# Kernel optimization log

Hardware: AMD Instinct MI355X
Metric: run time of the kernel (lower is better)

Reference implementation:

```python
import jax, jax.numpy as jnp
import numpy as np

B, LQ, LS, H = 4, 4096, 4096, 1024

def setup_inputs() -> dict:
    key = jax.random.key(0)
    k1, k2 = jax.random.split(key)
    query_input = jax.random.normal(k1, (B, LQ, H), dtype=jnp.float32)
    source_input = jax.random.normal(k2, (B, LS, H), dtype=jnp.float32)
    return {"query_input": query_input, "source_input": source_input}

def reference(query_input, source_input):
    # logits: [B, LQ, LS] = Q @ S^T, scaled by sqrt(d_k)
    dk = jnp.asarray(query_input.shape[-1], dtype=query_input.dtype)
    logits = jnp.einsum('bqh,bsh->bqs', query_input, source_input) / jnp.sqrt(dk)
    weights = jax.nn.softmax(logits, axis=-1)  # dropout inactive in eval mode
    # output: [B, LQ, H] = weights @ S (source doubles as values)
    return jnp.einsum('bqs,bsh->bqh', weights, source_input)
```

## Files before the change

### kernel.cpp

```cpp
#include <hip/hip_runtime.h>
#include <hip/hip_bf16.h>

#define B_   4
#define LQ_  4096
#define LS_  4096
#define DH_  1024
#define BQ_  64
#define BS_  256
#define NT_  (LS_/BS_)
#define NTH  512

typedef __bf16 bf16x8 __attribute__((ext_vector_type(8)));
typedef float  f32x4  __attribute__((ext_vector_type(4)));
typedef float  f32x16 __attribute__((ext_vector_type(16)));
typedef unsigned char u8;

#define WAITL()  asm volatile("s_waitcnt lgkmcnt(0)" ::: "memory")
#define BAR()    __builtin_amdgcn_s_barrier()

__device__ __forceinline__ unsigned short f2bf(float f) {
  union { __bf16 h; unsigned short u; } cv;
  cv.h = (__bf16)f;
  return cv.u;
}
__device__ __forceinline__ bf16x8 cvt8(f32x4 a, f32x4 b) {
  bf16x8 r;
  r[0] = (__bf16)a[0]; r[1] = (__bf16)a[1]; r[2] = (__bf16)a[2]; r[3] = (__bf16)a[3];
  r[4] = (__bf16)b[0]; r[5] = (__bf16)b[1]; r[6] = (__bf16)b[2]; r[7] = (__bf16)b[3];
  return r;
}

__global__ __launch_bounds__(256) void cvt_kernel(const float* __restrict__ S,
                                                  u8* __restrict__ Kf,
                                                  u8* __restrict__ Vf)
{
  __shared__ unsigned short tile[64][72];
  const int b  = blockIdx.z;
  const int dt = blockIdx.y;
  const int st = blockIdx.x;
  const int tid = threadIdx.x;
  const int t  = st >> 2;
  const float* Sbase = S + ((size_t)b*LS_ + (size_t)st*64)*DH_ + dt*64;

  #pragma unroll
  for (int k = 0; k < 4; ++k) {
    int fi  = tid + k*256;
    int row = fi >> 4;
    int c4  = fi & 15;
    float4 v = *reinterpret_cast<const float4*>(Sbase + (size_t)row*DH_ + c4*4);
    ushort4 h;
    h.x = f2bf(v.x); h.y = f2bf(v.y); h.z = f2bf(v.z); h.w = f2bf(v.w);
    *reinterpret_cast<ushort4*>(&tile[row][c4*4]) = h;
  }
  __syncthreads();

  #pragma unroll
  for (int h2 = 0; h2 < 2; ++h2) {
    int u    = tid + h2*256;
    int blk  = u >> 6;
    int wloc = blk >> 2;
    int kkl  = blk & 3;
    int lane = u & 63;
    int sh   = lane >> 5, sl = lane & 31;
    int srow = wloc*32 + sl;
    int scol = kkl*16 + sh*8;
    ushort4 h0 = *reinterpret_cast<const ushort4*>(&tile[srow][scol]);
    ushort4 h1 = *reinterpret_cast<const ushort4*>(&tile[srow][scol+4]);
    int w_g  = (st & 3)*2 + wloc;
    int kk_g = dt*4 + kkl;
    u8* dst = Kf + (size_t)(((b*16 + t)*8 + w_g)*64 + kk_g)*1024 + lane*16;
    *reinterpret_cast<ushort4*>(dst)     = h0;
    *reinterpret_cast<ushort4*>(dst + 8) = h1;
  }

  #pragma unroll
  for (int h2 = 0; h2 < 2; ++h2) {
    int u    = tid + h2*256;
    int blk  = u >> 6;
    int ksl  = blk >> 2;
    int nfl  = blk & 3;
    int lane = u & 63;
    int lg   = lane >> 4, lr = lane & 15;
    int srow = ksl*32 + lg*8;
    int dcol = nfl*16 + lr;
    ushort4 h0, h1;
    h0.x = tile[srow+0][dcol]; h0.y = tile[srow+1][dcol];
    h0.z = tile[srow+2][dcol]; h0.w = tile[srow+3][dcol];
    h1.x = tile[srow+4][dcol]; h1.y = tile[srow+5][dcol];
    h1.z = tile[srow+6][dcol]; h1.w = tile[srow+7][dcol];
    int w_g = dt >> 1;
    int i_g = ((st & 3)*2 + ksl)*8 + (dt & 1)*4 + nfl;
    u8* dst = Vf + (size_t)(((b*16 + t)*8 + w_g)*64 + i_g)*1024 + lane*16;
    *reinterpret_cast<ushort4*>(dst)     = h0;
    *reinterpret_cast<ushort4*>(dst + 8) = h1;
  }
}

__global__ __launch_bounds__(NTH, 2) void attn_kernel(
    const float* __restrict__ Qg,
    const u8* __restrict__ Kf,
    const u8* __restrict__ Vf,
    float* __restrict__ Og)
{
  __shared__ __align__(16) unsigned char qlds[131072];
  __shared__ __align__(16) unsigned char plds[32768];

  const int tid = threadIdx.x;
  const int w  = tid >> 6;
  const int l  = tid & 63;
  const int lg = l >> 4;
  const int lr = l & 15;
  const int sl = l & 31;
  const int sh = l >> 5;

  const int n    = blockIdx.x;
  const int xcd  = n & 7;
  const int slot = n >> 3;
  const int b    = xcd >> 1;
  const int qt   = (xcd & 1)*32 + slot;

  const float* Qbase = Qg + ((size_t)b*LQ_ + (size_t)qt*BQ_)*DH_;
  const u8* kptr = Kf + (size_t)b*8388608 + (size_t)w*65536 + l*16;
  const u8* vptr = Vf + (size_t)b*8388608 + (size_t)w*65536 + l*16;

  bf16x8 bk[4];
  auto ld_bk = [&](int t, int kk) -> bf16x8 {
    return *reinterpret_cast<const bf16x8*>(kptr + (size_t)t*524288 + kk*1024);
  };
  bf16x8 bv[4];
  auto ld_bv = [&](int t, int ks, int nf) -> bf16x8 {
    return *reinterpret_cast<const bf16x8*>(vptr + (size_t)t*524288 + (ks*8 + nf)*1024);
  };

  bk[0] = ld_bk(0, 0); bk[1] = ld_bk(0, 1); bk[2] = ld_bk(0, 2);

  #pragma unroll
  for (int it = 0; it < 16; ++it) {
    int u  = tid + it*NTH;
    int qf = u >> 12;
    int kk = (u >> 6) & 63;
    int ll = u & 63;
    int q  = qf*32 + (ll & 31);
    int d  = kk*16 + (ll >> 5)*8;
    const float* p = Qbase + (size_t)q*DH_ + d;
    f32x4 v0 = *reinterpret_cast<const f32x4*>(p);
    f32x4 v1 = *reinterpret_cast<const f32x4*>(p + 4);
    *reinterpret_cast<bf16x8*>(qlds + (size_t)u*16) = cvt8(v0, v1);
  }

  f32x4 Oacc[4][8];
  #pragma unroll
  for (int i = 0; i < 4; ++i)
    #pragma unroll
    for (int j = 0; j < 8; ++j)
      Oacc[i][j] = (f32x4){0.f, 0.f, 0.f, 0.f};
  f32x4 lacc[4];
  #pragma unroll
  for (int i = 0; i < 4; ++i) lacc[i] = (f32x4){0.f, 0.f, 0.f, 0.f};

  bf16x8 ones;
  #pragma unroll
  for (int e = 0; e < 8; ++e) ones[e] = (__bf16)1.0f;

  WAITL();
  BAR();

  for (int t = 0; t < NT_; ++t) {
    f32x16 qk0, qk1;
    #pragma unroll
    for (int r = 0; r < 16; ++r) { qk0[r] = 0.f; qk1[r] = 0.f; }

    bf16x8 aqA0 = *reinterpret_cast<const bf16x8*>(qlds + l*16);
    bf16x8 aqA1 = *reinterpret_cast<const bf16x8*>(qlds + 65536 + l*16);

    #pragma unroll
    for (int kk = 0; kk < 64; ++kk) {
      if (kk < 61) bk[(kk + 3) & 3] = ld_bk(t, kk + 3);
      bf16x8 aqN0, aqN1;
      if (kk < 63) {
        aqN0 = *reinterpret_cast<const bf16x8*>(qlds + (kk + 1)*1024 + l*16);
        aqN1 = *reinterpret_cast<const bf16x8*>(qlds + 65536 + (kk + 1)*1024 + l*16);
      }
      __builtin_amdgcn_s_setprio(1);
      qk0 = __builtin_amdgcn_mfma_f32_32x32x16_bf16(aqA0, bk[kk & 3], qk0, 0, 0, 0);
      qk1 = __builtin_amdgcn_mfma_f32_32x32x16_bf16(aqA1, bk[kk & 3], qk1, 0, 0, 0);
      __builtin_amdgcn_s_setprio(0);
      if (kk < 63) { aqA0 = aqN0; aqA1 = aqN1; }
    }

    const float SCL = 0.04508422f;
    #pragma unroll
    for (int r = 0; r < 16; ++r) {
      int qrow = (r & 3) + 8*(r >> 2) + 4*sh;
      int s    = w*32 + sl;
      {
        float p = exp2f(qk0[r] * SCL);
        int q = qrow;
        *reinterpret_cast<__bf16*>(plds + q*512 + ((s*2) ^ ((q & 7) << 4))) = (__bf16)p;
      }
      {
        float p = exp2f(qk1[r] * SCL);
        int q = 32 + qrow;
        *reinterpret_cast<__bf16*>(plds + q*512 + ((s*2) ^ ((q & 7) << 4))) = (__bf16)p;
      }
    }

    bv[0] = ld_bv(t, 0, 0); bv[1] = ld_bv(t, 0, 1); bv[2] = ld_bv(t, 0, 2);
    WAITL();
    BAR();

    bf16x8 pa0, pa1, pa2, pa3, pn0, pn1, pn2, pn3;
    auto ldP = [&](int mq, int ks) -> bf16x8 {
      int q = mq*16 + lr;
      return *reinterpret_cast<const bf16x8*>(
          plds + q*512 + ((ks*64 + lg*16) ^ ((q & 7) << 4)));
    };
    pa0 = ldP(0, 0); pa1 = ldP(1, 0); pa2 = ldP(2, 0); pa3 = ldP(3, 0);

    #pragma unroll
    for (int ks = 0; ks < 8; ++ks) {
      #pragma unroll
      for (int nf = 0; nf < 8; ++nf) {
        const int i = ks*8 + nf;
        if (i < 61) bv[(i + 3) & 3] = ld_bv(t, (i + 3) >> 3, (i + 3) & 7);
        if (t + 1 < NT_ && i >= 61) bk[i - 61] = ld_bk(t + 1, i - 61);
        if (ks < 7) {
          if (nf == 1) pn0 = ldP(0, ks + 1);
          if (nf == 2) pn1 = ldP(1, ks + 1);
          if (nf == 3) pn2 = ldP(2, ks + 1);
          if (nf == 4) pn3 = ldP(3, ks + 1);
        }
        if (nf == 0 && w == 0) {
          lacc[0] = __builtin_amdgcn_mfma_f32_16x16x32_bf16(pa0, ones, lacc[0], 0, 0, 0);
          lacc[1] = __builtin_amdgcn_mfma_f32_16x16x32_bf16(pa1, ones, lacc[1], 0, 0, 0);
          lacc[2] = __builtin_amdgcn_mfma_f32_16x16x32_bf16(pa2, ones, lacc[2], 0, 0, 0);
          lacc[3] = __builtin_amdgcn_mfma_f32_16x16x32_bf16(pa3, ones, lacc[3], 0, 0, 0);
        }
        __builtin_amdgcn_s_setprio(1);
        Oacc[0][nf] = __builtin_amdgcn_mfma_f32_16x16x32_bf16(pa0, bv[i & 3], Oacc[0][nf], 0, 0, 0);
        Oacc[1][nf] = __builtin_amdgcn_mfma_f32_16x16x32_bf16(pa1, bv[i & 3], Oacc[1][nf], 0, 0, 0);
        Oacc[2][nf] = __builtin_amdgcn_mfma_f32_16x16x32_bf16(pa2, bv[i & 3], Oacc[2][nf], 0, 0, 0);
        Oacc[3][nf] = __builtin_amdgcn_mfma_f32_16x16x32_bf16(pa3, bv[i & 3], Oacc[3][nf], 0, 0, 0);
        __builtin_amdgcn_s_setprio(0);
      }
      if (ks < 7) { pa0 = pn0; pa1 = pn1; pa2 = pn2; pa3 = pn3; }
    }
    BAR();
  }

  float* lred = (float*)plds;
  if (w == 0 && lr == 0) {
    #pragma unroll
    for (int mq = 0; mq < 4; ++mq)
      #pragma unroll
      for (int j = 0; j < 4; ++j)
        lred[mq*16 + lg*4 + j] = lacc[mq][j];
  }
  WAITL();
  BAR();

  float* Ob = Og + ((size_t)b*LQ_ + (size_t)qt*BQ_)*DH_;
  #pragma unroll
  for (int mq = 0; mq < 4; ++mq)
    #pragma unroll
    for (int j = 0; j < 4; ++j) {
      int q = mq*16 + lg*4 + j;
      float rinv = 1.0f / lred[q];
      #pragma unroll
      for (int nf = 0; nf < 8; ++nf)
        Ob[(size_t)q*DH_ + w*128 + nf*16 + lr] = Oacc[mq][nf][j] * rinv;
    }
}

__global__ void attn_naive(const float* __restrict__ Q, const float* __restrict__ S,
                           float* __restrict__ O)
{
  const int row = blockIdx.x;
  const int b = row >> 12, q = row & 4095;
  const float* qp = Q + ((size_t)b*LQ_ + q)*DH_;
  const float* sp = S + (size_t)b*LS_*DH_;
  __shared__ float qs[DH_];
  __shared__ float osum[DH_];
  __shared__ float lsum;
  for (int i = threadIdx.x; i < DH_; i += 256) { qs[i] = qp[i]; osum[i] = 0.f; }
  if (threadIdx.x == 0) lsum = 0.f;
  __syncthreads();
  float lpart = 0.f;
  for (int s0 = threadIdx.x; s0 < LS_; s0 += 256) {
    const float* sr = sp + (size_t)s0*DH_;
    float dot = 0.f;
    for (int d = 0; d < DH_; ++d) dot += qs[d]*sr[d];
    float p = __expf(dot * 0.03125f);
    lpart += p;
    for (int d = 0; d < DH_; ++d) atomicAdd(&osum[d], p*sr[d]);
  }
  atomicAdd(&lsum, lpart);
  __syncthreads();
  float rinv = 1.0f / lsum;
  float* op = O + ((size_t)b*LQ_ + q)*DH_;
  for (int i = threadIdx.x; i < DH_; i += 256) op[i] = osum[i]*rinv;
}

extern "C" void kernel_launch(void* const* d_in, const int* in_sizes, int n_in,
                              void* d_out, int out_size, void* d_ws, size_t ws_size,
                              hipStream_t stream)
{
  const float* Q = (const float*)d_in[0];
  const float* S = (const float*)d_in[1];
  float* out = (float*)d_out;

  const size_t kf_bytes = (size_t)B_*NT_*8*64*1024;
  const size_t vf_bytes = (size_t)B_*NT_*8*64*1024;
  const size_t need = kf_bytes + vf_bytes;

  if (ws_size >= need) {
    u8* Kf = (u8*)d_ws;
    u8* Vf = Kf + kf_bytes;
    cvt_kernel<<<dim3(64, 16, 4), 256, 0, stream>>>(S, Kf, Vf);
    attn_kernel<<<dim3(256), NTH, 0, stream>>>(Q, Kf, Vf, out);
  } else {
    attn_naive<<<dim3(B_*LQ_), 256, 0, stream>>>(Q, S, out);
  }
}
```

Baseline: 302.0 us.

## Software-pipeline QK^T of next tile with PV of previous tile in one loop

Restructures the main loop so the QK^T MFMAs for tile t are interleaved with the PV MFMAs for tile t-1. A prologue computes the first QK^T and an epilogue runs the final PV. It also drops the s_setprio hints and lowers launch_bounds occupancy from 2 to 1, giving more registers for the extra live accumulators. The goal is to hide the softmax/LDS barrier bubbles and load latency by overlapping the two matmul phases, at the cost of higher register pressure and lower occupancy.

Measured after the change: 347.7 us. 1.15x slower.

```diff
diff --git a/kernel.cpp b/kernel.cpp
--- a/kernel.cpp
+++ b/kernel.cpp
@@ -96,7 +96,7 @@
   }
 }
 
-__global__ __launch_bounds__(NTH, 2) void attn_kernel(
+__global__ __launch_bounds__(NTH, 1) void attn_kernel(
     const float* __restrict__ Qg,
     const u8* __restrict__ Kf,
     const u8* __restrict__ Vf,
@@ -128,8 +128,13 @@
     return *reinterpret_cast<const bf16x8*>(kptr + (size_t)t*524288 + kk*1024);
   };
   bf16x8 bv[4];
-  auto ld_bv = [&](int t, int ks, int nf) -> bf16x8 {
-    return *reinterpret_cast<const bf16x8*>(vptr + (size_t)t*524288 + (ks*8 + nf)*1024);
+  auto ld_bv = [&](int t, int i) -> bf16x8 {
+    return *reinterpret_cast<const bf16x8*>(vptr + (size_t)t*524288 + i*1024);
+  };
+  auto ldP = [&](int mq, int ks) -> bf16x8 {
+    int q = mq*16 + lr;
+    return *reinterpret_cast<const bf16x8*>(
+        plds + q*512 + ((ks*64 + lg*16) ^ ((q & 7) << 4)));
   };
 
   bk[0] = ld_bk(0, 0); bk[1] = ld_bk(0, 1); bk[2] = ld_bk(0, 2);
@@ -162,33 +167,34 @@
   #pragma unroll
   for (int e = 0; e < 8; ++e) ones[e] = (__bf16)1.0f;
 
+  f32x16 qk0, qk1;
+  const float SCL = 0.04508422f;
+
   WAITL();
   BAR();
 
-  for (int t = 0; t < NT_; ++t) {
-    f32x16 qk0, qk1;
-    #pragma unroll
-    for (int r = 0; r < 16; ++r) { qk0[r] = 0.f; qk1[r] = 0.f; }
-
+  #pragma unroll
+  for (int r = 0; r < 16; ++r) { qk0[r] = 0.f; qk1[r] = 0.f; }
+  {
     bf16x8 aqA0 = *reinterpret_cast<const bf16x8*>(qlds + l*16);
     bf16x8 aqA1 = *reinterpret_cast<const bf16x8*>(qlds + 65536 + l*16);
-
     #pragma unroll
     for (int kk = 0; kk < 64; ++kk) {
-      if (kk < 61) bk[(kk + 3) & 3] = ld_bk(t, kk + 3);
+      if (kk < 61) bk[(kk + 3) & 3] = ld_bk(0, kk + 3);
       bf16x8 aqN0, aqN1;
       if (kk < 63) {
         aqN0 = *reinterpret_cast<const bf16x8*>(qlds + (kk + 1)*1024 + l*16);
         aqN1 = *reinterpret_cast<const bf16x8*>(qlds + 65536 + (kk + 1)*1024 + l*16);
       }
-      __builtin_amdgcn_s_setprio(1);
       qk0 = __builtin_amdgcn_mfma_f32_32x32x16_bf16(aqA0, bk[kk & 3], qk0, 0, 0, 0);
       qk1 = __builtin_amdgcn_mfma_f32_32x32x16_bf16(aqA1, bk[kk & 3], qk1, 0, 0, 0);
-      __builtin_amdgcn_s_setprio(0);
       if (kk < 63) { aqA0 = aqN0; aqA1 = aqN1; }
     }
-
-    const float SCL = 0.04508422f;
+  }
+
+  for (int t = 1; t < NT_; ++t) {
+    BAR();
+
     #pragma unroll
     for (int r = 0; r < 16; ++r) {
       int qrow = (r & 3) + 8*(r >> 2) + 4*sh;
@@ -205,48 +211,91 @@
       }
     }
 
-    bv[0] = ld_bv(t, 0, 0); bv[1] = ld_bv(t, 0, 1); bv[2] = ld_bv(t, 0, 2);
+    bk[0] = ld_bk(t, 0); bk[1] = ld_bk(t, 1); bk[2] = ld_bk(t, 2);
+    bv[0] = ld_bv(t-1, 0); bv[1] = ld_bv(t-1, 1); bv[2] = ld_bv(t-1, 2);
+
     WAITL();
     BAR();
 
-    bf16x8 pa0, pa1, pa2, pa3, pn0, pn1, pn2, pn3;
-    auto ldP = [&](int mq, int ks) -> bf16x8 {
-      int q = mq*16 + lr;
-      return *reinterpret_cast<const bf16x8*>(
-          plds + q*512 + ((ks*64 + lg*16) ^ ((q & 7) << 4)));
-    };
-    pa0 = ldP(0, 0); pa1 = ldP(1, 0); pa2 = ldP(2, 0); pa3 = ldP(3, 0);
-
-    #pragma unroll
-    for (int ks = 0; ks < 8; ++ks) {
-      #pragma unroll
-      for (int nf = 0; nf < 8; ++nf) {
-        const int i = ks*8 + nf;
-        if (i < 61) bv[(i + 3) & 3] = ld_bv(t, (i + 3) >> 3, (i + 3) & 7);
-        if (t + 1 < NT_ && i >= 61) bk[i - 61] = ld_bk(t + 1, i - 61);
-        if (ks < 7) {
-          if (nf == 1) pn0 = ldP(0, ks + 1);
-          if (nf == 2) pn1 = ldP(1, ks + 1);
-          if (nf == 3) pn2 = ldP(2, ks + 1);
-          if (nf == 4) pn3 = ldP(3, ks + 1);
-        }
-        if (nf == 0 && w == 0) {
+    #pragma unroll
+    for (int r = 0; r < 16; ++r) { qk0[r] = 0.f; qk1[r] = 0.f; }
+
+    bf16x8 aqA0 = *reinterpret_cast<const bf16x8*>(qlds + l*16);
+    bf16x8 aqA1 = *reinterpret_cast<const bf16x8*>(qlds + 65536 + l*16);
+    bf16x8 pa0, pa1, pa2, pa3;
+
+    #pragma unroll
+    for (int i = 0; i < 64; ++i) {
+      const int ks = i >> 3, nf = i & 7;
+      if (i < 61) bk[(i + 3) & 3] = ld_bk(t, i + 3);
+      bf16x8 aqN0, aqN1;
+      if (i < 63) {
+        aqN0 = *reinterpret_cast<const bf16x8*>(qlds + (i + 1)*1024 + l*16);
+        aqN1 = *reinterpret_cast<const bf16x8*>(qlds + 65536 + (i + 1)*1024 + l*16);
+      }
+      qk0 = __builtin_amdgcn_mfma_f32_32x32x16_bf16(aqA0, bk[i & 3], qk0, 0, 0, 0);
+      qk1 = __builtin_amdgcn_mfma_f32_32x32x16_bf16(aqA1, bk[i & 3], qk1, 0, 0, 0);
+      if (i < 63) { aqA0 = aqN0; aqA1 = aqN1; }
+
+      if (i < 61) bv[(i + 3) & 3] = ld_bv(t-1, i + 3);
+      if (nf == 0) {
+        pa0 = ldP(0, ks); pa1 = ldP(1, ks); pa2 = ldP(2, ks); pa3 = ldP(3, ks);
+        if (w == 0) {
           lacc[0] = __builtin_amdgcn_mfma_f32_16x16x32_bf16(pa0, ones, lacc[0], 0, 0, 0);
           lacc[1] = __builtin_amdgcn_mfma_f32_16x16x32_bf16(pa1, ones, lacc[1], 0, 0, 0);
           lacc[2] = __builtin_amdgcn_mfma_f32_16x16x32_bf16(pa2, ones, lacc[2], 0, 0, 0);
           lacc[3] = __builtin_amdgcn_mfma_f32_16x16x32_bf16(pa3, ones, lacc[3], 0, 0, 0);
         }
-        __builtin_amdgcn_s_setprio(1);
-        Oacc[0][nf] = __builtin_amdgcn_mfma_f32_16x16x32_bf16(pa0, bv[i & 3], Oacc[0][nf], 0, 0, 0);
-        Oacc[1][nf] = __builtin_amdgcn_mfma_f32_16x16x32_bf16(pa1, bv[i & 3], Oacc[1][nf], 0, 0, 0);
-        Oacc[2][nf] = __builtin_amdgcn_mfma_f32_16x16x32_bf16(pa2, bv[i & 3], Oacc[2][nf], 0, 0, 0);
-        Oacc[3][nf] = __builtin_amdgcn_mfma_f32_16x16x32_bf16(pa3, bv[i & 3], Oacc[3][nf], 0, 0, 0);
-        __builtin_amdgcn_s_setprio(0);
-      }
-      if (ks < 7) { pa0 = pn0; pa1 = pn1; pa2 = pn2; pa3 = pn3; }
-    }
-    BAR();
-  }
+      }
+      Oacc[0][nf] = __builtin_amdgcn_mfma_f32_16x16x32_bf16(pa0, bv[i & 3], Oacc[0][nf], 0, 0, 0);
+      Oacc[1][nf] = __builtin_amdgcn_mfma_f32_16x16x32_bf16(pa1, bv[i & 3], Oacc[1][nf], 0, 0, 0);
+      Oacc[2][nf] = __builtin_amdgcn_mfma_f32_16x16x32_bf16(pa2, bv[i & 3], Oacc[2][nf], 0, 0, 0);
+      Oacc[3][nf] = __builtin_amdgcn_mfma_f32_16x16x32_bf16(pa3, bv[i & 3], Oacc[3][nf], 0, 0, 0);
+    }
+  }
+
+  BAR();
+  #pragma unroll
+  for (int r = 0; r < 16; ++r) {
+    int qrow = (r & 3) + 8*(r >> 2) + 4*sh;
+    int s    = w*32 + sl;
+    {
+      float p = exp2f(qk0[r] * SCL);
+      int q = qrow;
+      *reinterpret_cast<__bf16*>(plds + q*512 + ((s*2) ^ ((q & 7) << 4))) = (__bf16)p;
+    }
+    {
+      float p = exp2f(qk1[r] * SCL);
+      int q = 32 + qrow;
+      *reinterpret_cast<__bf16*>(plds + q*512 + ((s*2) ^ ((q & 7) << 4))) = (__bf16)p;
+    }
+  }
+  bv[0] = ld_bv(NT_-1, 0); bv[1] = ld_bv(NT_-1, 1); bv[2] = ld_bv(NT_-1, 2);
+  WAITL();
+  BAR();
+
+  {
+    bf16x8 pa0, pa1, pa2, pa3;
+    #pragma unroll
+    for (int i = 0; i < 64; ++i) {
+      const int ks = i >> 3, nf = i & 7;
+      if (i < 61) bv[(i + 3) & 3] = ld_bv(NT_-1, i + 3);
+      if (nf == 0) {
+        pa0 = ldP(0, ks); pa1 = ldP(1, ks); pa2 = ldP(2, ks); pa3 = ldP(3, ks);
+        if (w == 0) {
+          lacc[0] = __builtin_amdgcn_mfma_f32_16x16x32_bf16(pa0, ones, lacc[0], 0, 0, 0);
+          lacc[1] = __builtin_amdgcn_mfma_f32_16x16x32_bf16(pa1, ones, lacc[1], 0, 0, 0);
+          lacc[2] = __builtin_amdgcn_mfma_f32_16x16x32_bf16(pa2, ones, lacc[2], 0, 0, 0);
+          lacc[3] = __builtin_amdgcn_mfma_f32_16x16x32_bf16(pa3, ones, lacc[3], 0, 0, 0);
+        }
+      }
+      Oacc[0][nf] = __builtin_amdgcn_mfma_f32_16x16x32_bf16(pa0, bv[i & 3], Oacc[0][nf], 0, 0, 0);
+      Oacc[1][nf] = __builtin_amdgcn_mfma_f32_16x16x32_bf16(pa1, bv[i & 3], Oacc[1][nf], 0, 0, 0);
+      Oacc[2][nf] = __builtin_amdgcn_mfma_f32_16x16x32_bf16(pa2, bv[i & 3], Oacc[2][nf], 0, 0, 0);
+      Oacc[3][nf] = __builtin_amdgcn_mfma_f32_16x16x32_bf16(pa3, bv[i & 3], Oacc[3][nf], 0, 0, 0);
+    }
+  }
+  BAR();
 
   float* lred = (float*)plds;
   if (w == 0 && lr == 0) {
```
